# Kernel tuning notes

Hardware: AMD Instinct MI355X
Metric: run time of the kernel (lower is better)

Reference implementation:

```python
import jax, jax.numpy as jnp
import numpy as np


def conv1x1(x, W, b=None):
    # 1x1 conv == channel matmul: x (B,C,H,W), W (O,C)
    y = jnp.einsum('oc,bchw->bohw', W, x)
    if b is not None:
        y = y + b[None, :, None, None]
    return y


def setup_inputs() -> dict:
    key = jax.random.key(0)
    ks = jax.random.split(key, 20)
    B, C_l, C_h, H, W, d = 2, 64, 192, 64, 64, 128
    s = 0.02
    return {
        'll': jax.random.normal(ks[0], (B, C_l, H, W), jnp.float32),
        'hf': jax.random.normal(ks[1], (B, C_h, H, W), jnp.float32),
        'Wqh': jax.random.normal(ks[2], (d, C_h), jnp.float32) * s,
        'Wkh': jax.random.normal(ks[3], (d, C_h), jnp.float32) * s,
        'Wvh': jax.random.normal(ks[4], (d, C_h), jnp.float32) * s,
        'Wql': jax.random.normal(ks[5], (d, C_l), jnp.float32) * s,
        'Wkl': jax.random.normal(ks[6], (d, C_l), jnp.float32) * s,
        'Wvl': jax.random.normal(ks[7], (d, C_l), jnp.float32) * s,
        'Wph': jax.random.normal(ks[8], (C_h, d), jnp.float32) * s,
        'bph': jnp.zeros((C_h,), jnp.float32),
        'Wpl': jax.random.normal(ks[9], (C_l, d), jnp.float32) * s,
        'bpl': jnp.zeros((C_l,), jnp.float32),
        'Wah': jax.random.normal(ks[10], (C_h, C_h), jnp.float32) * s,
        'bah': jnp.zeros((C_h,), jnp.float32),
        'Wal': jax.random.normal(ks[11], (C_l, C_l), jnp.float32) * s,
        'bal': jnp.zeros((C_l,), jnp.float32),
        'alpha': jnp.ones((4,), jnp.float32),
    }


def reference(ll, hf, Wqh, Wkh, Wvh, Wql, Wkl, Wvl, Wph, bph, Wpl, bpl,
              Wah, bah, Wal, bal, alpha):
    B, C_l, H, W = ll.shape
    d = Wqh.shape[0]
    N = H * W
    scl = d ** (-0.5)

    Qh = conv1x1(hf, Wqh).reshape(B, d, N)
    Kh = conv1x1(hf, Wkh).reshape(B, d, N)
    Vh = conv1x1(hf, Wvh).reshape(B, d, N)
    Ql = conv1x1(ll, Wql).reshape(B, d, N)
    Kl = conv1x1(ll, Wkl).reshape(B, d, N)
    Vl = conv1x1(ll, Wvl).reshape(B, d, N)

    wdir = jax.nn.softmax(alpha)  # [row, col, diag, global]

    def sdpa(q, k, v):  # q,k,v: (B, L, d)
        a = jax.nn.softmax(jnp.einsum('bqd,bkd->bqk', q, k) * scl, axis=-1)
        return jnp.einsum('bqk,bkd->bqd', a, v)

    # ---- global: full N x N cross attention ----
    OL = sdpa(Qh.transpose(0, 2, 1), Kl.transpose(0, 2, 1), Vl.transpose(0, 2, 1)).transpose(0, 2, 1)
    OH = sdpa(Ql.transpose(0, 2, 1), Kh.transpose(0, 2, 1), Vh.transpose(0, 2, 1)).transpose(0, 2, 1)
    out_ll = conv1x1(OL.reshape(B, d, H, W), Wpl, bpl) * wdir[3]
    out_hf = conv1x1(OH.reshape(B, d, H, W), Wph, bph) * wdir[3]

    # ---- axial (row / col) attention ----
    def axial(q, k, v, row):
        perm = (0, 2, 3, 1) if row else (0, 3, 2, 1)  # (B,S,L,d)
        qr = q.reshape(B, d, H, W).transpose(perm)
        kr = k.reshape(B, d, H, W).transpose(perm)
        vr = v.reshape(B, d, H, W).transpose(perm)
        a = jax.nn.softmax(jnp.einsum('bsqd,bskd->bsqk', qr, kr) * scl, axis=-1)
        o = jnp.einsum('bsqk,bskd->bsqd', a, vr)
        inv = (0, 3, 1, 2) if row else (0, 3, 2, 1)
        return o.transpose(inv)  # (B,d,H,W)

    out_ll = out_ll + conv1x1(axial(Qh, Kl, Vl, True), Wpl, bpl) * wdir[0]
    out_hf = out_hf + conv1x1(axial(Ql, Kh, Vh, True), Wph, bph) * wdir[0]
    out_ll = out_ll + conv1x1(axial(Qh, Kl, Vl, False), Wpl, bpl) * wdir[1]
    out_hf = out_hf + conv1x1(axial(Ql, Kh, Vh, False), Wph, bph) * wdir[1]

    # ---- diag: faithful to original code (gather by diag index, attend, scatter back) ----
    i = jnp.arange(H)[:, None]
    j = jnp.arange(W)[None, :]
    flat_idx = (j - i + (H - 1)).reshape(-1)  # (N,), values in [0, H+W-2]

    def dsel(x):  # (B,d,N) -> (B,N,d) gathered along position axis
        return x[:, :, flat_idx].transpose(0, 2, 1)

    Ld = sdpa(dsel(Qh), dsel(Kl), dsel(Vl)).transpose(0, 2, 1)  # (B,d,N)
    Hd = sdpa(dsel(Ql), dsel(Kh), dsel(Vh)).transpose(0, 2, 1)
    blank_l = jnp.zeros((B, d, N), Ld.dtype).at[:, :, flat_idx].set(Ld)
    blank_h = jnp.zeros((B, d, N), Hd.dtype).at[:, :, flat_idx].set(Hd)
    out_ll = out_ll + conv1x1(blank_l.reshape(B, d, H, W), Wpl, bpl) * wdir[2]
    out_hf = out_hf + conv1x1(blank_h.reshape(B, d, H, W), Wph, bph) * wdir[2]

    ll_out = conv1x1(ll + out_ll, Wal, bal)
    hf_out = conv1x1(hf + out_hf, Wah, bah)
    return (ll_out, hf_out)
```

## Files before the change

### kernel.cpp

```cpp
#include <hip/hip_runtime.h>
#include <math.h>

#define N_  4096
#define D_  128
#define B_  2
#define CL_ 64
#define CH_ 192

typedef __attribute__((ext_vector_type(8))) short short8;
typedef __attribute__((ext_vector_type(4))) float f32x4;
typedef __attribute__((ext_vector_type(16))) float f32x16;

#if __has_builtin(__builtin_amdgcn_exp2f)
#define EXP2(x) __builtin_amdgcn_exp2f(x)
#else
#define EXP2(x) exp2f(x)
#endif

__device__ __forceinline__ short f2bf(float x) {
  union { float f; unsigned u; } v; v.f = x;
  unsigned r = v.u + 0x7FFFu + ((v.u >> 16) & 1u);
  return (short)(r >> 16);
}

typedef __attribute__((address_space(1))) const void gv_t;
typedef __attribute__((address_space(3))) void sv_t;
__device__ __forceinline__ void gl_lds16(const void* g, void* l) {
  __builtin_amdgcn_global_load_lds((gv_t*)g, (sv_t*)l, 16, 0, 0);
}

#define CVTPK(d, lo, hi) asm("v_cvt_pk_bf16_f32 %0, %1, %2" : "=v"(d) : "v"(lo), "v"(hi))
#define PLSWAP(a, b) asm("v_permlane32_swap_b32 %0, %1" : "+v"(a), "+v"(b))

__global__ __launch_bounds__(256)
void xt_kernel(const float* __restrict__ hf, const float* __restrict__ ll,
               short* __restrict__ hfT, short* __restrict__ llT) {
  __shared__ float Ls[CH_][65];
  const int tid = threadIdx.x;
  const int n0 = blockIdx.x * 64;
  const int b = blockIdx.y;
  const int s = blockIdx.z;
  const int C = s ? CL_ : CH_;
  const float* src = (s ? ll : hf) + (size_t)b * C * N_;
  short* dst = (s ? llT : hfT) + (size_t)b * N_ * C;
  for (int flat = tid; flat < C * 64; flat += 256) {
    int c = flat >> 6, nn = flat & 63;
    Ls[c][nn] = src[(size_t)c * N_ + n0 + nn];
  }
  __syncthreads();
  const int ng = C >> 3;
  for (int u = tid; u < 64 * ng; u += 256) {
    int nn = u / ng, g = u - nn * ng;
    short8 v;
    #pragma unroll
    for (int j = 0; j < 8; ++j) v[j] = f2bf(Ls[g*8 + j][nn]);
    int pos = (g & ~7) | ((g ^ (nn & 7)) & 7);
    *(short8*)(dst + (size_t)(n0 + nn) * C + pos * 8) = v;
  }
}

__global__ __launch_bounds__(256)
void vt_kernel(const short* __restrict__ Vhb, const short* __restrict__ Vlb,
               short* __restrict__ Vht, short* __restrict__ Vlt) {
  __shared__ short rowbuf[4 * 4096];
  const int tid = threadIdx.x;
  const int lane = tid & 63, w = tid >> 6;
  const short* src = blockIdx.y ? Vlb : Vhb;
  short* dst = blockIdx.y ? Vlt : Vht;
  const int r0 = blockIdx.x * 4;
  #pragma unroll
  for (int i = 0; i < 8; ++i) {
    int idx = i * 256 + w * 64 + lane;
    int row = idx >> 9, g = idx & 511;
    gl_lds16(src + (size_t)(r0 + row) * N_ + g * 8,
             (char*)rowbuf + i * 4096 + w * 1024 + lane * 16);
  }
  __syncthreads();
  const int rw = r0 + w, d7 = rw & 7;
  const short* rb = rowbuf + w * 4096;
  const int w0 = (lane & 7) * 8, h0 = (lane >> 3) * 8;
  short8 rr[8];
  #pragma unroll
  for (int j = 0; j < 8; ++j)
    rr[j] = *(const short8*)(rb + (h0 + j) * 64 + (((w0 >> 3) ^ d7) * 8));
  #pragma unroll
  for (int i = 0; i < 8; ++i) {
    short8 o;
    #pragma unroll
    for (int j = 0; j < 8; ++j) o[j] = rr[j][i];
    *(short8*)(dst + (size_t)rw * N_ + (w0 + i) * 64 + (((h0 >> 3) ^ d7) * 8)) = o;
  }
}

struct QkvP {
  const float *W0h, *W1h, *W2h, *W0l, *W1l, *W2l;
  const short *BsH, *BsL;
  short *QbH, *KbH, *VbH, *QtH, *KtH;
  short *QbL, *KbL, *VbL, *QtL, *KtL;
  float qscale;
};

__global__ __launch_bounds__(256, 4)
void qkv_kernel(QkvP g) {
  __shared__ __align__(16) char AB[16384];
  __shared__ float Epi[64][67];
  const int tid = threadIdx.x;
  const int lane = tid & 63, w = tid >> 6, m = lane & 15, hi = lane >> 4;
  const int n0 = blockIdx.x * 64;
  const int sel = blockIdx.y >> 1, dhalf = blockIdx.y & 1, ot0 = dhalf * 64;
  const int b = blockIdx.z >> 1, s = blockIdx.z & 1;
  const int C = s ? CL_ : CH_;
  const float* Wm = s ? (sel == 0 ? g.W0l : sel == 1 ? g.W1l : g.W2l)
                      : (sel == 0 ? g.W0h : sel == 1 ? g.W1h : g.W2h);
  const short* Bs = (s ? g.BsL : g.BsH) + (size_t)b * N_ * C;

  f32x4 acc[4];
  #pragma unroll
  for (int i = 0; i < 4; ++i) acc[i] = (f32x4){0.f, 0.f, 0.f, 0.f};

  for (int c0 = 0; c0 < C; c0 += 64) {
    __syncthreads();
    {
      int o = tid >> 2, cq = tid & 3;
      const float* wp = Wm + (size_t)(ot0 + o) * C + c0 + cq * 16;
      float4 fa = *(const float4*)(wp + 0);
      float4 fb = *(const float4*)(wp + 4);
      float4 fc = *(const float4*)(wp + 8);
      float4 fd = *(const float4*)(wp + 12);
      short8 v0 = { f2bf(fa.x), f2bf(fa.y), f2bf(fa.z), f2bf(fa.w),
                    f2bf(fb.x), f2bf(fb.y), f2bf(fb.z), f2bf(fb.w) };
      short8 v1 = { f2bf(fc.x), f2bf(fc.y), f2bf(fc.z), f2bf(fc.w),
                    f2bf(fd.x), f2bf(fd.y), f2bf(fd.z), f2bf(fd.w) };
      int g0 = cq * 2;
      *(short8*)(AB + o * 128 + (((g0) ^ (o & 7)) * 16)) = v0;
      *(short8*)(AB + o * 128 + (((g0 + 1) ^ (o & 7)) * 16)) = v1;
    }
    #pragma unroll
    for (int e = 0; e < 2; ++e) {
      int cid = e * 256 + w * 64 + lane;
      int nn = cid >> 3, gs = cid & 7;
      gl_lds16(Bs + (size_t)(n0 + nn) * C + c0 + gs * 8,
               AB + 8192 + e * 4096 + w * 1024 + lane * 16);
    }
    __syncthreads();
    const int orow = w * 16 + m;
    short8 a0 = *(const short8*)(AB + orow * 128 + (((hi) ^ (orow & 7)) * 16));
    short8 a1 = *(const short8*)(AB + orow * 128 + (((4 + hi) ^ (orow & 7)) * 16));
    #pragma unroll
    for (int nf = 0; nf < 4; ++nf) {
      int nrow = nf * 16 + m;
      short8 b0 = *(const short8*)(AB + 8192 + nrow * 128 + (((hi) ^ (nrow & 7)) * 16));
      short8 b1 = *(const short8*)(AB + 8192 + nrow * 128 + (((4 + hi) ^ (nrow & 7)) * 16));
      acc[nf] = __builtin_amdgcn_mfma_f32_16x16x32_bf16(a0, b0, acc[nf], 0, 0, 0);
      acc[nf] = __builtin_amdgcn_mfma_f32_16x16x32_bf16(a1, b1, acc[nf], 0, 0, 0);
    }
  }

  #pragma unroll
  for (int nf = 0; nf < 4; ++nf)
    #pragma unroll
    for (int r = 0; r < 4; ++r)
      Epi[w * 16 + hi * 4 + r][nf * 16 + m] = acc[nf][r];
  __syncthreads();

  if (sel < 2) {
    float sc = (sel == 0) ? g.qscale : 1.f;
    short* QK = (sel == 0 ? (s ? g.QbL : g.QbH) : (s ? g.KbL : g.KbH)) + (size_t)b * N_ * D_;
    short* QKt = (sel == 0 ? (s ? g.QtL : g.QtH) : (s ? g.KtL : g.KtH)) + (size_t)b * N_ * D_;
    const int bx = blockIdx.x;
    #pragma unroll
    for (int e = 0; e < 2; ++e) {
      int u = tid + 256 * e;
      int nn = u >> 3, gl = u & 7;
      short8 v;
      #pragma unroll
      for (int j = 0; j < 8; ++j) v[j] = f2bf(Epi[gl*8 + j][nn] * sc);
      int posb = (dhalf * 8) | ((gl ^ (nn & 7)) & 7);
      *(short8*)(QK + (size_t)(n0 + nn) * D_ + posb * 8) = v;
      int post = (dhalf * 8) | ((gl ^ (bx & 7)) & 7);
      *(short8*)(QKt + (size_t)(nn * 64 + bx) * D_ + post * 8) = v;
    }
  } else {
    short* Vb = (s ? g.VbL : g.VbH) + (size_t)b * D_ * N_;
    #pragma unroll
    for (int e = 0; e < 2; ++e) {
      int u = tid + 256 * e;
      int o = u >> 3, gl = u & 7;
      int d = ot0 + o;
      short8 v;
      #pragma unroll
      for (int j = 0; j < 8; ++j) v[j] = f2bf(Epi[o][gl*8 + j]);
      *(short8*)(Vb + (size_t)d * N_ + n0 + ((gl ^ (d & 7)) * 8)) = v;
    }
  }
}

struct SmP {
  const short *Qhb, *Qlb, *Khb, *Klb, *Vhb, *Vlb;
  const short *Qht, *Qlt, *Kht, *Klt, *Vht, *Vlt;
  float *Mrl, *Mrh, *Mcl, *Mch, *Mdl, *Mdh;
  const float* alpha;
};

__global__ __launch_bounds__(256, 2)
void attn_sm(SmP p) {
  __shared__ __align__(16) char smem[49152];
  const int tid = threadIdx.x;
  const int lane = tid & 63, w = tid >> 6, m = lane & 15, hi = lane >> 4;

  const int bxg = blockIdx.x;
  int variant, y, bz, qx;
  if (bxg < 256)      { variant = 0; y = bxg & 63;        bz = bxg >> 6;        qx = 0; }
  else if (bxg < 512) { variant = 1; y = (bxg-256) & 63;  bz = (bxg-256) >> 6;  qx = 0; }
  else                { variant = 2; y = 0;               bz = (bxg-512) >> 1;  qx = (bxg-512) & 1; }
  const int b = bz >> 1, pair = bz & 1;
  const int widx = variant;
  const int cwflag = (variant == 2);
  const int qbase = (variant == 2) ? qx * 64 : y * 64;
  const int kcol0 = (variant == 2) ? 0 : y * 64;
  const int Lk = (variant == 2) ? 127 : 64;
  const int lqloc = (variant == 2) ? (qx ? 63 : 64) : 64;

  const short *Qs, *Ks, *Vs;
  if (variant == 1) {
    Qs = pair ? p.Qlt : p.Qht; Ks = pair ? p.Kht : p.Klt; Vs = pair ? p.Vht : p.Vlt;
  } else {
    Qs = pair ? p.Qlb : p.Qhb; Ks = pair ? p.Khb : p.Klb; Vs = pair ? p.Vhb : p.Vlb;
  }
  Qs += (size_t)b * N_ * D_; Ks += (size_t)b * N_ * D_; Vs += (size_t)b * D_ * N_;
  float* Mout;
  if (variant == 0)      Mout = (pair ? p.Mrh : p.Mrl) + (size_t)b * D_ * N_;
  else if (variant == 1) Mout = (pair ? p.Mch : p.Mcl) + (size_t)b * D_ * N_;
  else                   Mout = (pair ? p.Mdh : p.Mdl) + (size_t)b * D_ * 128;

  float a0 = p.alpha[0], a1 = p.alpha[1], a2 = p.alpha[2], a3 = p.alpha[3];
  float am = fmaxf(fmaxf(a0, a1), fmaxf(a2, a3));
  float e0 = __expf(a0-am), e1 = __expf(a1-am), e2 = __expf(a2-am), e3 = __expf(a3-am);
  float wsel = (widx == 0 ? e0 : widx == 1 ? e1 : e2) / (e0 + e1 + e2 + e3);

  auto stageK = [&](int kt) {
    #pragma unroll
    for (int i = 0; i < 4; ++i) {
      int chunk = w * 4 + i;
      gl_lds16(Ks + (size_t)(kcol0 + kt*64) * D_ + chunk * 512 + lane * 8,
               smem + 16384 + chunk * 1024);
    }
  };
  auto stageV = [&](int kt) {
    #pragma unroll
    for (int i = 0; i < 4; ++i) {
      int chunk = w * 4 + i;
      gl_lds16(Vs + (size_t)(chunk*8 + (lane>>3)) * N_ + kcol0 + kt*64 + (lane&7)*8,
               smem + 32768 + chunk * 1024);
    }
  };
  #pragma unroll
  for (int i = 0; i < 4; ++i) {
    int chunk = w * 4 + i;
    gl_lds16(Qs + (size_t)qbase * D_ + chunk * 512 + lane * 8, smem + chunk * 1024);
  }
  stageK(0); stageV(0);
  __syncthreads();

  const int qrow = w * 16 + m;
  short8 qf[4];
  #pragma unroll
  for (int cs = 0; cs < 4; ++cs)
    qf[cs] = *(const short8*)(smem + qrow * 256 + ((cs*64 + hi*16) ^ ((qrow & 7) << 4)));
  __syncthreads();

  f32x4 oacc[8];
  #pragma unroll
  for (int i = 0; i < 8; ++i) oacc[i] = (f32x4){0.f, 0.f, 0.f, 0.f};
  float m_run[4] = {-INFINITY, -INFINITY, -INFINITY, -INFINITY};
  float l_run[4] = {0.f, 0.f, 0.f, 0.f};
  char* const pstrip = smem + w * 2048;
  const int NT = (Lk + 63) >> 6;

  for (int kt = 0; kt < NT; ++kt) {
    const char* Kc = smem + 16384;
    const char* Vc = smem + 32768;
    f32x4 sacc[4];
    #pragma unroll
    for (int kf = 0; kf < 4; ++kf) sacc[kf] = (f32x4){0.f, 0.f, 0.f, 0.f};
    #pragma unroll
    for (int kf = 0; kf < 4; ++kf) {
      const int krow = kf * 16 + m;
      const char* kr = Kc + krow * 256;
      #pragma unroll
      for (int cs = 0; cs < 4; ++cs) {
        short8 kfr = *(const short8*)(kr + ((cs*64 + hi*16) ^ ((krow & 7) << 4)));
        sacc[kf] = __builtin_amdgcn_mfma_f32_16x16x32_bf16(qf[cs], kfr, sacc[kf], 0, 0, 0);
      }
    }
    float cw[4];
    #pragma unroll
    for (int kf = 0; kf < 4; ++kf) {
      if (cwflag) {
        int kg = kt * 64 + kf * 16 + m;
        int dd = kg - 63; dd = dd < 0 ? -dd : dd;
        cw[kf] = (kg < Lk) ? (float)(64 - dd) : 0.f;
      } else cw[kf] = 1.f;
    }
    #pragma unroll
    for (int r = 0; r < 4; ++r) {
      float mt = fmaxf(fmaxf(sacc[0][r], sacc[1][r]), fmaxf(sacc[2][r], sacc[3][r]));
      mt = fmaxf(mt, __shfl_xor(mt, 1));
      mt = fmaxf(mt, __shfl_xor(mt, 2));
      mt = fmaxf(mt, __shfl_xor(mt, 4));
      mt = fmaxf(mt, __shfl_xor(mt, 8));
      float mn = fmaxf(m_run[r], mt);
      float corr = EXP2(m_run[r] - mn);
      m_run[r] = mn;
      const int rl = hi * 4 + r;
      char* prow = pstrip + rl * 128;
      float psum = 0.f;
      #pragma unroll
      for (int kf = 0; kf < 4; ++kf) {
        float pv = cw[kf] * EXP2(sacc[kf][r] - mn);
        psum += pv;
        int kcol = (kf * 16 + m) * 2;
        *(short*)(prow + (kcol ^ ((rl & 7) << 4))) = f2bf(pv);
      }
      psum += __shfl_xor(psum, 1);
      psum += __shfl_xor(psum, 2);
      psum += __shfl_xor(psum, 4);
      psum += __shfl_xor(psum, 8);
      l_run[r] = l_run[r] * corr + psum;
      #pragma unroll
      for (int cf = 0; cf < 8; ++cf) oacc[cf][r] *= corr;
    }
    #pragma unroll
    for (int ks = 0; ks < 2; ++ks) {
      short8 pa = *(const short8*)(pstrip + m * 128 + ((ks*64 + hi*16) ^ ((m & 7) << 4)));
      #pragma unroll
      for (int cf = 0; cf < 8; ++cf) {
        const int crow = cf * 16 + m;
        short8 vf = *(const short8*)(Vc + crow * 128 + ((ks*64 + hi*16) ^ ((crow & 7) << 4)));
        oacc[cf] = __builtin_amdgcn_mfma_f32_16x16x32_bf16(pa, vf, oacc[cf], 0, 0, 0);
      }
    }
    __syncthreads();
    if (kt + 1 < NT) { stageK(kt + 1); stageV(kt + 1); __syncthreads(); }
  }

  float inv[4];
  #pragma unroll
  for (int r = 0; r < 4; ++r) inv[r] = wsel / l_run[r];
  float* Os = (float*)smem;
  #pragma unroll
  for (int cf = 0; cf < 8; ++cf)
    #pragma unroll
    for (int r = 0; r < 4; ++r)
      Os[(cf*16 + m) * 66 + w * 16 + hi * 4 + r] = oacc[cf][r] * inv[r];
  __syncthreads();
  for (int it = 0; it < 32; ++it) {
    int flat = it * 256 + tid;
    int c = flat >> 6, qq = flat & 63;
    if (qq < lqloc) {
      float v = Os[c * 66 + qq];
      if (variant == 0)      Mout[(size_t)c * N_ + qbase + qq] = v;
      else if (variant == 1) Mout[(size_t)c * N_ + qq * 64 + y] = v;
      else                   Mout[c * 128 + qbase + qq] = v;
    }
  }
}

#define GVQ 65536

struct GlobalAttnParams {
  const short *Qhb, *Qlb, *Khb, *Klb, *Vhb, *Vlb;
  const float *Mrl, *Mrh, *Mcl, *Mch, *Mdl, *Mdh;
  short *Mtbl, *Mtbh;
  const float* alpha;
};

__global__ __launch_bounds__(512, 1)
void attn_gl_kernel(GlobalAttnParams p) {
  __shared__ __align__(16) char smem[131072];
  const int tid = threadIdx.x;
  const int lane = tid & 63, w = tid >> 6;
  const int wid = w & 1, gsel = w >> 1;
  const int key = lane & 31, kh = lane >> 5;

  const int bx = blockIdx.x;
  const int xcd = bx & 7, sub = bx >> 3;
  const int pz = xcd >> 1;
  const int b = pz >> 1, pair = pz & 1;
  const int q0 = ((xcd & 1) * 32 + sub) * 64;

  const short* Qb = (pair ? p.Qlb : p.Qhb) + (size_t)b * N_ * D_;
  const short* Kb = (pair ? p.Khb : p.Klb) + (size_t)b * N_ * D_;
  const short* Vb = (pair ? p.Vhb : p.Vlb) + (size_t)b * D_ * N_;
  const float* Mr = (pair ? p.Mrh : p.Mrl) + (size_t)b * D_ * N_;
  const float* Mc = (pair ? p.Mch : p.Mcl) + (size_t)b * D_ * N_;
  const float* Md = (pair ? p.Mdh : p.Mdl) + (size_t)b * D_ * 128;
  short* Mtb = (pair ? p.Mtbh : p.Mtbl) + (size_t)b * N_ * D_;

  float a0 = p.alpha[0], a1 = p.alpha[1], a2 = p.alpha[2], a3 = p.alpha[3];
  float am = fmaxf(fmaxf(a0,a1), fmaxf(a2,a3));
  float e0 = __expf(a0-am), e1 = __expf(a1-am), e2 = __expf(a2-am), e3 = __expf(a3-am);
  const float wsel = e3 / (e0+e1+e2+e3);

  auto stageQuad = [&](int qd) {
    #pragma unroll
    for (int i = 0; i < 8; ++i) {
      int c = w*8 + i;
      if (c < 32) {
        int tk = c >> 3, ck = c & 7;
        gl_lds16(Kb + (size_t)((4*qd + tk)*32 + ck*4)*D_ + lane*8,
                 smem + (qd & 1)*32768 + tk*8192 + ck*1024);
      } else {
        int cc = c - 32;
        int d = cc*4 + (lane >> 4);
        int g = lane & 15, kb2 = g >> 3, gg = g & 7;
        gl_lds16(Vb + (size_t)d*N_ + qd*128 + kb2*64 + ((gg ^ (d & 7))*8),
                 smem + GVQ + (qd & 1)*32768 + cc*1024);
      }
    }
  };

  const int qq = wid*32 + key;
  const short* qrow_g = Qb + (size_t)(q0 + qq) * D_;
  short8 qf[8];
  #pragma unroll
  for (int fi = 0; fi < 8; ++fi)
    qf[fi] = *(const short8*)(qrow_g + (((fi*2 + kh) ^ (qq & 7)) << 3));

  stageQuad(0);

  f32x16 oacc[4];
  #pragma unroll
  for (int d = 0; d < 4; ++d)
    #pragma unroll
    for (int r = 0; r < 16; ++r) oacc[d][r] = 0.f;
  float m_run = -INFINITY, l_run = 0.f;

  const int NQ = N_ / 128;
  for (int j = 0; j < NQ; ++j) {
    __syncthreads();
    if (j + 1 < NQ) stageQuad(j + 1);

    const char* Kc = smem + (j & 1)*32768 + gsel*8192;
    const char* Vc = smem + GVQ + (j & 1)*32768;

    f32x16 sacc;
    #pragma unroll
    for (int r = 0; r < 16; ++r) sacc[r] = 0.f;
    __builtin_amdgcn_s_setprio(1);
    #pragma unroll
    for (int fi = 0; fi < 8; ++fi) {
      short8 kf = *(const short8*)(Kc + key*256 + (((fi*2 + kh) ^ (key & 7)) << 4));
      sacc = __builtin_amdgcn_mfma_f32_32x32x16_bf16(kf, qf[fi], sacc, 0, 0, 0);
    }
    __builtin_amdgcn_s_setprio(0);

    float mt = sacc[0];
    #pragma unroll
    for (int r = 1; r < 16; ++r) mt = fmaxf(mt, sacc[r]);
    { float aa = mt, bb = mt; PLSWAP(aa, bb); mt = fmaxf(aa, bb); }
    if (!__all(mt <= m_run + 8.f)) {
      float mn = fmaxf(m_run, mt);
      float corr = EXP2(m_run - mn);
      m_run = mn;
      l_run *= corr;
      #pragma unroll
      for (int d = 0; d < 4; ++d)
        #pragma unroll
        for (int r = 0; r < 16; ++r) oacc[d][r] *= corr;
    }
    float pv[16];
    float psum = 0.f;
    #pragma unroll
    for (int r = 0; r < 16; ++r) { pv[r] = EXP2(sacc[r] - m_run); psum += pv[r]; }
    { float sa = psum, sb = psum; PLSWAP(sa, sb); psum = sa + sb; }
    l_run += psum;

    union U8 { unsigned u[4]; short8 s; } pf0, pf1;
    {
      unsigned c0, c1, c2, c3;
      CVTPK(c0, pv[0], pv[1]);  CVTPK(c1, pv[2], pv[3]);
      CVTPK(c2, pv[4], pv[5]);  CVTPK(c3, pv[6], pv[7]);
      PLSWAP(c0, c2); PLSWAP(c1, c3);
      pf0.u[0] = c0; pf0.u[1] = c1; pf0.u[2] = c2; pf0.u[3] = c3;
      CVTPK(c0, pv[8],  pv[9]);  CVTPK(c1, pv[10], pv[11]);
      CVTPK(c2, pv[12], pv[13]); CVTPK(c3, pv[14], pv[15]);
      PLSWAP(c0, c2); PLSWAP(c1, c3);
      pf1.u[0] = c0; pf1.u[1] = c1; pf1.u[2] = c2; pf1.u[3] = c3;
    }

    __builtin_amdgcn_s_setprio(1);
    #pragma unroll
    for (int d = 0; d < 4; ++d) {
      #pragma unroll
      for (int ks = 0; ks < 2; ++ks) {
        int crow = d*32 + key;
        int gidx = gsel*4 + ks*2 + kh;
        int kb2 = gidx >> 3, gg = gidx & 7;
        short8 vf = *(const short8*)(Vc + crow*256 + kb2*128 + ((gg ^ (key & 7)) << 4));
        oacc[d] = __builtin_amdgcn_mfma_f32_32x32x16_bf16(vf, (ks ? pf1.s : pf0.s), oacc[d], 0, 0, 0);
      }
    }
    __builtin_amdgcn_s_setprio(0);
  }
  __syncthreads();

  float* MLbase = (float*)(smem + 98304);
  if (gsel > 0) {
    int idx = (gsel - 1)*2 + wid;
    float* ob = (float*)smem + idx*4096;
    #pragma unroll
    for (int d = 0; d < 4; ++d)
      #pragma unroll
      for (int r = 0; r < 16; ++r)
        ob[(d*16 + r)*64 + lane] = oacc[d][r];
    float* ml = MLbase + idx*128;
    ml[lane] = m_run;
    ml[64 + lane] = l_run;
  }
  __syncthreads();

  float inv = 0.f;
  if (gsel == 0) {
    float mp[3], lp[3];
    float mn = m_run;
    #pragma unroll
    for (int pi = 0; pi < 3; ++pi) {
      const float* ml = MLbase + (pi*2 + wid)*128;
      mp[pi] = ml[lane]; lp[pi] = ml[64 + lane];
      mn = fmaxf(mn, mp[pi]);
    }
    float cA = EXP2(m_run - mn);
    float lt = l_run * cA;
    #pragma unroll
    for (int d = 0; d < 4; ++d)
      #pragma unroll
      for (int r = 0; r < 16; ++r) oacc[d][r] *= cA;
    #pragma unroll
    for (int pi = 0; pi < 3; ++pi) {
      float cp = EXP2(mp[pi] - mn);
      lt += lp[pi] * cp;
      const float* ob = (const float*)smem + (pi*2 + wid)*4096;
      #pragma unroll
      for (int d = 0; d < 4; ++d)
        #pragma unroll
        for (int r = 0; r < 16; ++r)
          oacc[d][r] += ob[(d*16 + r)*64 + lane] * cp;
    }
    inv = wsel / lt;
  }
  __syncthreads();

  float* Os = (float*)smem;
  if (gsel == 0) {
    #pragma unroll
    for (int d = 0; d < 4; ++d)
      #pragma unroll
      for (int r = 0; r < 16; ++r) {
        int dr = d*32 + (r & 3) + 8*(r >> 2) + 4*kh;
        Os[dr*66 + qq] = oacc[d][r] * inv;
      }
  }
  __syncthreads();

  for (int it = 0; it < 16; ++it) {
    int flat = it*512 + tid;
    int c = flat >> 6, q2 = flat & 63;
    int pos = q0 + q2;
    float add = Mr[(size_t)c*N_ + pos] + Mc[(size_t)c*N_ + pos];
    if (pos < 127) add += Md[c*128 + pos];
    Os[c*66 + q2] += add;
  }
  __syncthreads();
  #pragma unroll
  for (int e = 0; e < 2; ++e) {
    int u = tid + 512*e;
    int nn = u >> 4, gb = u & 15;
    short8 v;
    #pragma unroll
    for (int jj = 0; jj < 8; ++jj) v[jj] = f2bf(Os[(gb*8 + jj)*66 + nn]);
    int pos = (gb & 8) | ((gb ^ (nn & 7)) & 7);
    *(short8*)(Mtb + (size_t)(q0 + nn)*D_ + pos*8) = v;
  }
}

struct Gemm2P {
  const float *WA; const short *BA; const float *resA, *biasA; float *outA; short *UtA; int KA, OA;
  const float *WB; const short *BB; const float *resB, *biasB; float *outB; short *UtB; int KB, OB;
  int ysplit, epmode;
};

__global__ __launch_bounds__(256, 4)
void gemm2_bf16(Gemm2P g) {
  __shared__ __align__(16) char AB[16384];
  __shared__ float Epi[64][67];
  const int tid = threadIdx.x;
  const int lane = tid & 63, w = tid >> 6, m = lane & 15, hi = lane >> 4;
  const int n0 = blockIdx.x * 64;
  const int b = blockIdx.z;
  const int yy = blockIdx.y;
  const bool isB = yy >= g.ysplit;
  const int ot0 = (isB ? (yy - g.ysplit) : yy) * 64;
  const float* Wm = isB ? g.WB : g.WA;
  const int K = isB ? g.KB : g.KA;
  const int O = isB ? g.OB : g.OA;
  const short* Bs = (isB ? g.BB : g.BA) + (size_t)b * N_ * K;

  f32x4 acc[4];
  #pragma unroll
  for (int i = 0; i < 4; ++i) acc[i] = (f32x4){0.f, 0.f, 0.f, 0.f};

  for (int c0 = 0; c0 < K; c0 += 64) {
    __syncthreads();
    {
      int o = tid >> 2, cq = tid & 3;
      const float* wp = Wm + (size_t)(ot0 + o) * K + c0 + cq * 16;
      float4 fa = *(const float4*)(wp + 0);
      float4 fb = *(const float4*)(wp + 4);
      float4 fc = *(const float4*)(wp + 8);
      float4 fd = *(const float4*)(wp + 12);
      short8 v0 = { f2bf(fa.x), f2bf(fa.y), f2bf(fa.z), f2bf(fa.w),
                    f2bf(fb.x), f2bf(fb.y), f2bf(fb.z), f2bf(fb.w) };
      short8 v1 = { f2bf(fc.x), f2bf(fc.y), f2bf(fc.z), f2bf(fc.w),
                    f2bf(fd.x), f2bf(fd.y), f2bf(fd.z), f2bf(fd.w) };
      int g0 = cq * 2;
      *(short8*)(AB + o * 128 + (((g0) ^ (o & 7)) * 16)) = v0;
      *(short8*)(AB + o * 128 + (((g0 + 1) ^ (o & 7)) * 16)) = v1;
    }
    #pragma unroll
    for (int e = 0; e < 2; ++e) {
      int cid = e * 256 + w * 64 + lane;
      int nn = cid >> 3, gs = cid & 7;
      gl_lds16(Bs + (size_t)(n0 + nn) * K + c0 + gs * 8,
               AB + 8192 + e * 4096 + w * 1024 + lane * 16);
    }
    __syncthreads();
    const int orow = w * 16 + m;
    short8 a0 = *(const short8*)(AB + orow * 128 + (((hi) ^ (orow & 7)) * 16));
    short8 a1 = *(const short8*)(AB + orow * 128 + (((4 + hi) ^ (orow & 7)) * 16));
    #pragma unroll
    for (int nf = 0; nf < 4; ++nf) {
      int nrow = nf * 16 + m;
      short8 b0 = *(const short8*)(AB + 8192 + nrow * 128 + (((hi) ^ (nrow & 7)) * 16));
      short8 b1 = *(const short8*)(AB + 8192 + nrow * 128 + (((4 + hi) ^ (nrow & 7)) * 16));
      acc[nf] = __builtin_amdgcn_mfma_f32_16x16x32_bf16(a0, b0, acc[nf], 0, 0, 0);
      acc[nf] = __builtin_amdgcn_mfma_f32_16x16x32_bf16(a1, b1, acc[nf], 0, 0, 0);
    }
  }

  #pragma unroll
  for (int nf = 0; nf < 4; ++nf)
    #pragma unroll
    for (int r = 0; r < 4; ++r)
      Epi[w * 16 + hi * 4 + r][nf * 16 + m] = acc[nf][r];
  __syncthreads();

  if (g.epmode == 1) {
    const float* res = (isB ? g.resB : g.resA) + (size_t)b * O * N_;
    const float* bias = isB ? g.biasB : g.biasA;
    short* Ut = (isB ? g.UtB : g.UtA) + (size_t)b * N_ * O;
    #pragma unroll
    for (int e = 0; e < 2; ++e) {
      int nn = tid & 63;
      int gl = (tid >> 6) + e * 4;
      int ob = ot0 + gl * 8;
      short8 v;
      #pragma unroll
      for (int j = 0; j < 8; ++j)
        v[j] = f2bf(Epi[gl*8 + j][nn] + res[(size_t)(ob + j) * N_ + n0 + nn] + bias[ob + j]);
      int gout = (ot0 >> 3) + gl;
      int pos = (gout & ~7) | ((gout ^ (nn & 7)) & 7);
      *(short8*)(Ut + (size_t)(n0 + nn) * O + pos * 8) = v;
    }
  } else {
    const float* bias = isB ? g.biasB : g.biasA;
    float* outF = isB ? g.outB : g.outA;
    int o = tid >> 2, nq = tid & 3;
    float bv = bias[ot0 + o];
    float* dst = outF + (size_t)b * O * N_ + (size_t)(ot0 + o) * N_ + n0 + nq * 16;
    #pragma unroll
    for (int q4 = 0; q4 < 4; ++q4) {
      float4 vv = { Epi[o][nq*16 + q4*4 + 0] + bv, Epi[o][nq*16 + q4*4 + 1] + bv,
                    Epi[o][nq*16 + q4*4 + 2] + bv, Epi[o][nq*16 + q4*4 + 3] + bv };
      *(float4*)(dst + q4 * 4) = vv;
    }
  }
}

extern "C" void kernel_launch(void* const* d_in, const int* in_sizes, int n_in,
                              void* d_out, int out_size, void* d_ws, size_t ws_size,
                              hipStream_t stream) {
  (void)in_sizes; (void)n_in; (void)out_size; (void)ws_size;
  const float* ll  = (const float*)d_in[0];
  const float* hf  = (const float*)d_in[1];
  const float* Wqh = (const float*)d_in[2];
  const float* Wkh = (const float*)d_in[3];
  const float* Wvh = (const float*)d_in[4];
  const float* Wql = (const float*)d_in[5];
  const float* Wkl = (const float*)d_in[6];
  const float* Wvl = (const float*)d_in[7];
  const float* Wph = (const float*)d_in[8];
  const float* bph = (const float*)d_in[9];
  const float* Wpl = (const float*)d_in[10];
  const float* bpl = (const float*)d_in[11];
  const float* Wah = (const float*)d_in[12];
  const float* bah = (const float*)d_in[13];
  const float* Wal = (const float*)d_in[14];
  const float* bal = (const float*)d_in[15];
  const float* alpha = (const float*)d_in[16];

  float* ws = (float*)d_ws;
  const size_t BDN = (size_t)B_ * D_ * N_;
  float* Mrl = ws;
  float* Mrh = Mrl + BDN;
  float* Mcl = Mrh + BDN;
  float* Mch = Mcl + BDN;
  float* Mdl = Mch + BDN;
  float* Mdh = Mdl + (size_t)B_ * D_ * 128;
  short* sp = (short*)(Mdh + (size_t)B_ * D_ * 128);
  short* Qhb = sp;           sp += BDN;
  short* Qlb = sp;           sp += BDN;
  short* Khb = sp;           sp += BDN;
  short* Klb = sp;           sp += BDN;
  short* Vhb = sp;           sp += BDN;
  short* Vlb = sp;           sp += BDN;
  short* Qht = sp;           sp += BDN;
  short* Qlt = sp;           sp += BDN;
  short* Kht = sp;           sp += BDN;
  short* Klt = sp;           sp += BDN;
  short* Vht = sp;           sp += BDN;
  short* Vlt = sp;           sp += BDN;
  short* hfT = sp;           sp += (size_t)B_ * N_ * CH_;
  short* llT = sp;           sp += (size_t)B_ * N_ * CL_;
  short* Mtbl = Qht;
  short* Mtbh = Qlt;
  short* Utl  = Kht;
  short* Uth  = Klt;

  dim3 blk(256, 1, 1);
  const float qscale = (float)(0.08838834764831845 * 1.4426950408889634);
  float* out = (float*)d_out;

  xt_kernel<<<dim3(N_/64, B_, 2), blk, 0, stream>>>(hf, ll, hfT, llT);

  QkvP qp{Wqh, Wkh, Wvh, Wql, Wkl, Wvl, hfT, llT,
          Qhb, Khb, Vhb, Qht, Kht, Qlb, Klb, Vlb, Qlt, Klt, qscale};
  qkv_kernel<<<dim3(N_/64, 6, 2*B_), blk, 0, stream>>>(qp);

  vt_kernel<<<dim3(64, 2), blk, 0, stream>>>(Vhb, Vlb, Vht, Vlt);

  SmP smp{Qhb, Qlb, Khb, Klb, Vhb, Vlb, Qht, Qlt, Kht, Klt, Vht, Vlt,
          Mrl, Mrh, Mcl, Mch, Mdl, Mdh, alpha};
  attn_sm<<<dim3(520, 1, 1), blk, 0, stream>>>(smp);

  GlobalAttnParams gp{Qhb, Qlb, Khb, Klb, Vhb, Vlb,
                      Mrl, Mrh, Mcl, Mch, Mdl, Mdh, Mtbl, Mtbh, alpha};
  attn_gl_kernel<<<dim3(256, 1, 1), dim3(512,1,1), 0, stream>>>(gp);

  Gemm2P wp{Wpl, Mtbl, ll, bpl, nullptr, Utl, D_, CL_,
            Wph, Mtbh, hf, bph, nullptr, Uth, D_, CH_, 1, 1};
  gemm2_bf16<<<dim3(N_/64, 4, B_), blk, 0, stream>>>(wp);

  Gemm2P wa{Wal, Utl, nullptr, bal, out, nullptr, CL_, CL_,
            Wah, Uth, nullptr, bah, out + (size_t)B_*CL_*N_, nullptr, CH_, CH_, 1, 2};
  gemm2_bf16<<<dim3(N_/64, 4, B_), blk, 0, stream>>>(wa);
}
```

Measured before the change: 123.0 us.

## Fuse input transpose/bf16 conversion into QKV projection kernel

Removes the separate xt_kernel that transposed fp32 inputs into bf16 channel-last buffers. The qkv kernel now reads fp32 activations directly, transposes them through LDS into a per-block bf16 tile covering all channels, and runs the MFMA loop from that tile. This saves one kernel launch and a global round trip of the transposed inputs. In exchange, each of the 6 projection blocks per tile repeats the transpose work and uses more LDS, so occupancy drops from 4 to 2 blocks.

After: 119.3 us. 3.0% less time.

```diff
diff --git a/kernel.cpp b/kernel.cpp
--- a/kernel.cpp
+++ b/kernel.cpp
@@ -31,33 +31,6 @@
 
 #define CVTPK(d, lo, hi) asm("v_cvt_pk_bf16_f32 %0, %1, %2" : "=v"(d) : "v"(lo), "v"(hi))
 #define PLSWAP(a, b) asm("v_permlane32_swap_b32 %0, %1" : "+v"(a), "+v"(b))
-
-__global__ __launch_bounds__(256)
-void xt_kernel(const float* __restrict__ hf, const float* __restrict__ ll,
-               short* __restrict__ hfT, short* __restrict__ llT) {
-  __shared__ float Ls[CH_][65];
-  const int tid = threadIdx.x;
-  const int n0 = blockIdx.x * 64;
-  const int b = blockIdx.y;
-  const int s = blockIdx.z;
-  const int C = s ? CL_ : CH_;
-  const float* src = (s ? ll : hf) + (size_t)b * C * N_;
-  short* dst = (s ? llT : hfT) + (size_t)b * N_ * C;
-  for (int flat = tid; flat < C * 64; flat += 256) {
-    int c = flat >> 6, nn = flat & 63;
-    Ls[c][nn] = src[(size_t)c * N_ + n0 + nn];
-  }
-  __syncthreads();
-  const int ng = C >> 3;
-  for (int u = tid; u < 64 * ng; u += 256) {
-    int nn = u / ng, g = u - nn * ng;
-    short8 v;
-    #pragma unroll
-    for (int j = 0; j < 8; ++j) v[j] = f2bf(Ls[g*8 + j][nn]);
-    int pos = (g & ~7) | ((g ^ (nn & 7)) & 7);
-    *(short8*)(dst + (size_t)(n0 + nn) * C + pos * 8) = v;
-  }
-}
 
 __global__ __launch_bounds__(256)
 void vt_kernel(const short* __restrict__ Vhb, const short* __restrict__ Vlb,
@@ -94,16 +67,17 @@
 
 struct QkvP {
   const float *W0h, *W1h, *W2h, *W0l, *W1l, *W2l;
-  const short *BsH, *BsL;
+  const float *Xh, *Xl;
   short *QbH, *KbH, *VbH, *QtH, *KtH;
   short *QbL, *KbL, *VbL, *QtL, *KtL;
   float qscale;
 };
 
-__global__ __launch_bounds__(256, 4)
+__global__ __launch_bounds__(256, 2)
 void qkv_kernel(QkvP g) {
-  __shared__ __align__(16) char AB[16384];
-  __shared__ float Epi[64][67];
+  __shared__ __align__(16) char BT[24576];
+  __shared__ __align__(16) char AS[8192];
+  __shared__ __align__(16) float Ls[64][67];
   const int tid = threadIdx.x;
   const int lane = tid & 63, w = tid >> 6, m = lane & 15, hi = lane >> 4;
   const int n0 = blockIdx.x * 64;
@@ -112,7 +86,29 @@
   const int C = s ? CL_ : CH_;
   const float* Wm = s ? (sel == 0 ? g.W0l : sel == 1 ? g.W1l : g.W2l)
                       : (sel == 0 ? g.W0h : sel == 1 ? g.W1h : g.W2h);
-  const short* Bs = (s ? g.BsL : g.BsH) + (size_t)b * N_ * C;
+  const float* Xs = (s ? g.Xl : g.Xh) + (size_t)b * C * N_;
+  const int C2 = C * 2;
+
+  for (int cc = 0; cc < C; cc += 64) {
+    #pragma unroll
+    for (int r = 0; r < 16; ++r) {
+      int flat = r * 256 + tid;
+      int c = flat >> 6, nn = flat & 63;
+      Ls[c][nn] = Xs[(size_t)(cc + c) * N_ + n0 + nn];
+    }
+    __syncthreads();
+    #pragma unroll
+    for (int e = 0; e < 2; ++e) {
+      int u = e * 256 + tid;
+      int nn = u >> 3, gl = u & 7;
+      short8 v;
+      #pragma unroll
+      for (int j = 0; j < 8; ++j) v[j] = f2bf(Ls[gl*8 + j][nn]);
+      int pos = (gl ^ (nn & 7)) & 7;
+      *(short8*)(BT + nn * C2 + cc * 2 + pos * 16) = v;
+    }
+    __syncthreads();
+  }
 
   f32x4 acc[4];
   #pragma unroll
@@ -132,35 +128,30 @@
       short8 v1 = { f2bf(fc.x), f2bf(fc.y), f2bf(fc.z), f2bf(fc.w),
                     f2bf(fd.x), f2bf(fd.y), f2bf(fd.z), f2bf(fd.w) };
       int g0 = cq * 2;
-      *(short8*)(AB + o * 128 + (((g0) ^ (o & 7)) * 16)) = v0;
-      *(short8*)(AB + o * 128 + (((g0 + 1) ^ (o & 7)) * 16)) = v1;
-    }
-    #pragma unroll
-    for (int e = 0; e < 2; ++e) {
-      int cid = e * 256 + w * 64 + lane;
-      int nn = cid >> 3, gs = cid & 7;
-      gl_lds16(Bs + (size_t)(n0 + nn) * C + c0 + gs * 8,
-               AB + 8192 + e * 4096 + w * 1024 + lane * 16);
+      *(short8*)(AS + o * 128 + (((g0) ^ (o & 7)) * 16)) = v0;
+      *(short8*)(AS + o * 128 + (((g0 + 1) ^ (o & 7)) * 16)) = v1;
     }
     __syncthreads();
     const int orow = w * 16 + m;
-    short8 a0 = *(const short8*)(AB + orow * 128 + (((hi) ^ (orow & 7)) * 16));
-    short8 a1 = *(const short8*)(AB + orow * 128 + (((4 + hi) ^ (orow & 7)) * 16));
+    short8 a0 = *(const short8*)(AS + orow * 128 + (((hi) ^ (orow & 7)) * 16));
+    short8 a1 = *(const short8*)(AS + orow * 128 + (((4 + hi) ^ (orow & 7)) * 16));
     #pragma unroll
     for (int nf = 0; nf < 4; ++nf) {
       int nrow = nf * 16 + m;
-      short8 b0 = *(const short8*)(AB + 8192 + nrow * 128 + (((hi) ^ (nrow & 7)) * 16));
-      short8 b1 = *(const short8*)(AB + 8192 + nrow * 128 + (((4 + hi) ^ (nrow & 7)) * 16));
+      const char* brow = BT + nrow * C2 + c0 * 2;
+      short8 b0 = *(const short8*)(brow + (((hi) ^ (nrow & 7)) * 16));
+      short8 b1 = *(const short8*)(brow + (((4 + hi) ^ (nrow & 7)) * 16));
       acc[nf] = __builtin_amdgcn_mfma_f32_16x16x32_bf16(a0, b0, acc[nf], 0, 0, 0);
       acc[nf] = __builtin_amdgcn_mfma_f32_16x16x32_bf16(a1, b1, acc[nf], 0, 0, 0);
     }
   }
 
+  __syncthreads();
   #pragma unroll
   for (int nf = 0; nf < 4; ++nf)
     #pragma unroll
     for (int r = 0; r < 4; ++r)
-      Epi[w * 16 + hi * 4 + r][nf * 16 + m] = acc[nf][r];
+      Ls[w * 16 + hi * 4 + r][nf * 16 + m] = acc[nf][r];
   __syncthreads();
 
   if (sel < 2) {
@@ -174,7 +165,7 @@
       int nn = u >> 3, gl = u & 7;
       short8 v;
       #pragma unroll
-      for (int j = 0; j < 8; ++j) v[j] = f2bf(Epi[gl*8 + j][nn] * sc);
+      for (int j = 0; j < 8; ++j) v[j] = f2bf(Ls[gl*8 + j][nn] * sc);
       int posb = (dhalf * 8) | ((gl ^ (nn & 7)) & 7);
       *(short8*)(QK + (size_t)(n0 + nn) * D_ + posb * 8) = v;
       int post = (dhalf * 8) | ((gl ^ (bx & 7)) & 7);
@@ -189,7 +180,7 @@
       int d = ot0 + o;
       short8 v;
       #pragma unroll
-      for (int j = 0; j < 8; ++j) v[j] = f2bf(Epi[o][gl*8 + j]);
+      for (int j = 0; j < 8; ++j) v[j] = f2bf(Ls[o][gl*8 + j]);
       *(short8*)(Vb + (size_t)d * N_ + n0 + ((gl ^ (d & 7)) * 8)) = v;
     }
   }
@@ -730,8 +721,6 @@
   short* Klt = sp;           sp += BDN;
   short* Vht = sp;           sp += BDN;
   short* Vlt = sp;           sp += BDN;
-  short* hfT = sp;           sp += (size_t)B_ * N_ * CH_;
-  short* llT = sp;           sp += (size_t)B_ * N_ * CL_;
   short* Mtbl = Qht;
   short* Mtbh = Qlt;
   short* Utl  = Kht;
@@ -741,9 +730,7 @@
   const float qscale = (float)(0.08838834764831845 * 1.4426950408889634);
   float* out = (float*)d_out;
 
-  xt_kernel<<<dim3(N_/64, B_, 2), blk, 0, stream>>>(hf, ll, hfT, llT);
-
-  QkvP qp{Wqh, Wkh, Wvh, Wql, Wkl, Wvl, hfT, llT,
+  QkvP qp{Wqh, Wkh, Wvh, Wql, Wkl, Wvl, hf, ll,
           Qhb, Khb, Vhb, Qht, Kht, Qlb, Klb, Vlb, Qlt, Klt, qscale};
   qkv_kernel<<<dim3(N_/64, 6, 2*B_), blk, 0, stream>>>(qp);
 
```
